# Kernel tuning notes

Hardware: AMD Instinct MI355X
Metric: run time of the kernel (lower is better)

The kernel has to match this reference:

```python
import jax, jax.numpy as jnp
import numpy as np

B, T, D = 2, 1024, 1024
E, H, TOPK = 32, 256, 4
S, HS = 2, H * TOPK  # shared experts, shared hidden dim


def setup_inputs() -> dict:
    key = jax.random.key(0)
    ks = jax.random.split(key, 10)
    sc = 0.02
    return {
        "x": jax.random.normal(ks[0], (B, T, D), dtype=jnp.float32),
        "Wr": jax.random.normal(ks[1], (E, D), dtype=jnp.float32) * sc,
        "router_bias": jnp.zeros((E,), dtype=jnp.float32),
        "Wg": jax.random.normal(ks[2], (E, H, D), dtype=jnp.float32) * sc,
        "Wu": jax.random.normal(ks[3], (E, H, D), dtype=jnp.float32) * sc,
        "Wd": jax.random.normal(ks[4], (E, D, H), dtype=jnp.float32) * sc,
        "Sg": jax.random.normal(ks[5], (S, HS, D), dtype=jnp.float32) * sc,
        "Su": jax.random.normal(ks[6], (S, HS, D), dtype=jnp.float32) * sc,
        "Sd": jax.random.normal(ks[7], (S, D, HS), dtype=jnp.float32) * sc,
    }


def reference(x, Wr, router_bias, Wg, Wu, Wd, Sg, Su, Sd):
    Bx, Tx, Dx = x.shape
    flat = x.reshape(-1, Dx)                      # [N, D]
    N = flat.shape[0]

    # Router: softmax over raw logits, top-k selection on biased logits
    logits = flat @ Wr.T                          # [N, E]
    scores = jax.nn.softmax(logits, axis=-1)
    _, topk_idx = jax.lax.top_k(logits + router_bias, TOPK)   # [N, K]
    topk_scores = jnp.take_along_axis(scores, topk_idx, axis=-1)
    topk_scores = topk_scores / jnp.sum(topk_scores, axis=-1, keepdims=True)

    # Dense per-token per-expert combine weights (0 for unselected experts)
    cw = jnp.zeros((N, E), dtype=flat.dtype).at[
        jnp.arange(N)[:, None], topk_idx
    ].add(topk_scores)                            # [N, E]

    # Routed experts: SwiGLU applied per expert, zero-weighted if unselected
    g = jnp.einsum("nd,ehd->neh", flat, Wg)       # [N, E, H]
    u = jnp.einsum("nd,ehd->neh", flat, Wu)
    h = jax.nn.silu(g) * u
    hw = h * cw[:, :, None]                       # fold combine weight before down-proj
    out = jnp.einsum("neh,edh->nd", hw, Wd)       # [N, D]

    # Shared experts: always active, summed on top
    gs = jnp.einsum("nd,shd->nsh", flat, Sg)      # [N, S, HS]
    us = jnp.einsum("nd,shd->nsh", flat, Su)
    hs = jax.nn.silu(gs) * us
    out = out + jnp.einsum("nsh,sdh->nd", hs, Sd)

    return out.reshape(Bx, Tx, Dx)
```

## Files before the change

kernel.cpp:

```cpp
#include <hip/hip_runtime.h>
#include <hip/hip_bf16.h>


#define N_TOK 2048
#define DDIM 1024
#define NEXP 32
#define HDIM 256
#define TOPK 4
#define NSH 2
#define HSH 1024
#define CNTS 32
#define WMAX 160

typedef unsigned short us4 __attribute__((ext_vector_type(4)));
typedef unsigned short us8 __attribute__((ext_vector_type(8)));
typedef short bf16x8 __attribute__((ext_vector_type(8)));
typedef float f32x4 __attribute__((ext_vector_type(4)));

__device__ __forceinline__ unsigned short f2bf(float f) {
  union { float f; unsigned u; } v; v.f = f;
  unsigned r = v.u + 0x7fffu + ((v.u >> 16) & 1u);
  return (unsigned short)(r >> 16);
}
__device__ __forceinline__ float bf2f(unsigned short h) {
  union { unsigned u; float f; } v; v.u = ((unsigned)h) << 16; return v.f;
}
__device__ __forceinline__ uint2 cvt4u(float4 v) {
  union { __hip_bfloat162 b; unsigned u; } a, b2;
  a.b  = __float22bfloat162_rn(make_float2(v.x, v.y));
  b2.b = __float22bfloat162_rn(make_float2(v.z, v.w));
  return make_uint2(a.u, b2.u);
}

__device__ __forceinline__ void pipe_barrier() {
  asm volatile("s_waitcnt lgkmcnt(0)" ::: "memory");
  __builtin_amdgcn_s_barrier();
  __builtin_amdgcn_sched_barrier(0);
}

#define C_X4   524288L
#define C_WG4  2621440L
#define C_WU4  4718592L
#define C_WD4  6815744L
#define C_SG4  7340032L
#define C_SU4  7864320L
#define C_TOT4 8388608L
#define NCVT   16384

__global__ __launch_bounds__(256) void k_prep(const float* __restrict__ x,
                                              const float* __restrict__ Wr,
                                              const float* __restrict__ rb,
                                              const float* __restrict__ Wg,
                                              const float* __restrict__ Wu,
                                              const float* __restrict__ Wd,
                                              const float* __restrict__ Sg,
                                              const float* __restrict__ Su,
                                              const float* __restrict__ Sd,
                                              unsigned short* __restrict__ xb,
                                              unsigned short* __restrict__ Wgb,
                                              unsigned short* __restrict__ Wub,
                                              unsigned short* __restrict__ Wdb,
                                              unsigned short* __restrict__ Sgb,
                                              unsigned short* __restrict__ Sub,
                                              unsigned short* __restrict__ Sdb,
                                              int* __restrict__ cnt,
                                              int* __restrict__ ent,
                                              float* __restrict__ wgt) {
  __shared__ float sX[8 * 1024];
  __shared__ float sLog[8 * 32];
  int tid = threadIdx.x;
  if (blockIdx.x >= 256) {
    long base = (long)(blockIdx.x - 256) * 512;
    const float* s; unsigned short* d; long off;
    if (base < C_WG4) {
      if (base < C_X4)  { s = x;  d = xb;  off = base; }
      else              { s = Wg; d = Wgb; off = base - C_X4; }
    } else if (base < C_WD4) {
      if (base < C_WU4) { s = Wu; d = Wub; off = base - C_WG4; }
      else              { s = Wd; d = Wdb; off = base - C_WU4; }
    } else if (base < C_SU4) {
      if (base < C_SG4) { s = Sg; d = Sgb; off = base - C_WD4; }
      else              { s = Su; d = Sub; off = base - C_SG4; }
    } else              { s = Sd; d = Sdb; off = base - C_SU4; }
    long i0 = off + tid;
    long i1 = i0 + 256;
    float4 v0 = reinterpret_cast<const float4*>(s)[i0];
    float4 v1 = reinterpret_cast<const float4*>(s)[i1];
    reinterpret_cast<uint2*>(d)[i0] = cvt4u(v0);
    reinterpret_cast<uint2*>(d)[i1] = cvt4u(v1);
    return;
  }
  int blk = blockIdx.x;
  {
    const float4* xsrc = reinterpret_cast<const float4*>(x + (size_t)blk * 8 * 1024);
    float4* xdst = reinterpret_cast<float4*>(sX);
#pragma unroll
    for (int i = 0; i < 8; i++) xdst[tid + 256 * i] = xsrc[tid + 256 * i];
  }
  __syncthreads();
  int tloc = tid >> 5, e = tid & 31;
  const float4* wr4 = reinterpret_cast<const float4*>(Wr + (size_t)e * DDIM);
  const float* xr = sX + tloc * 1024;
  float acc = 0.f;
#pragma unroll 8
  for (int d4 = 0; d4 < 256; d4++) {
    float4 wv = wr4[d4];
    acc += xr[d4 * 4 + 0] * wv.x + xr[d4 * 4 + 1] * wv.y +
           xr[d4 * 4 + 2] * wv.z + xr[d4 * 4 + 3] * wv.w;
  }
  sLog[tloc * 32 + e] = acc;
  __syncthreads();
  if (tid < 8) {
    int tok = blk * 8 + tid;
    const float* lg = sLog + tid * 32;
    int usedmask = 0;
    int idx[TOPK]; float lv[TOPK];
#pragma unroll
    for (int k = 0; k < TOPK; k++) {
      float best = -3.4e38f; int bi = 0;
      for (int ee = 0; ee < NEXP; ee++) {
        if ((usedmask >> ee) & 1) continue;
        float v = lg[ee] + rb[ee];
        if (v > best) { best = v; bi = ee; }
      }
      usedmask |= 1 << bi; idx[k] = bi; lv[k] = lg[bi];
    }
    float m = fmaxf(fmaxf(lv[0], lv[1]), fmaxf(lv[2], lv[3]));
    float w[TOPK]; float ssum = 0.f;
#pragma unroll
    for (int k = 0; k < TOPK; k++) { w[k] = __expf(lv[k] - m); ssum += w[k]; }
    float inv = 1.f / ssum;
#pragma unroll
    for (int k = 0; k < TOPK; k++) {
      int ee = idx[k];
      int pos = atomicAdd(&cnt[ee * CNTS], 1);
      ent[ee * N_TOK + pos] = tok * TOPK + k;
      wgt[ee * N_TOK + pos] = w[k] * inv;
    }
  }
}

__global__ void k_plan(const int* __restrict__ cnt, int* __restrict__ wk, int* __restrict__ nwk) {
  if (threadIdx.x != 0) return;
  int w = 0;
  for (int e = 0; e < NEXP; e++) {
    int ne = cnt[e * CNTS];
    int nt = (ne + 63) >> 6;
    for (int t = 0; t < nt; t++) wk[w++] = e | (t << 8);
  }
  nwk[0] = w;
}

__global__ __launch_bounds__(256) void k_routed_gu(const unsigned short* __restrict__ xb,
                                                   const unsigned short* __restrict__ Wgb,
                                                   const unsigned short* __restrict__ Wub,
                                                   const int* __restrict__ cnt,
                                                   const int* __restrict__ ent,
                                                   const float* __restrict__ wgt,
                                                   unsigned short* __restrict__ hw,
                                                   const int* __restrict__ wk,
                                                   const int* __restrict__ nwk) {
  int widx = blockIdx.x;
  if (widx >= nwk[0]) return;
  int item = wk[widx];
  int e = item & 255, mt = item >> 8, ht = blockIdx.y;
  int ne = cnt[e * CNTS];
  __shared__ unsigned short sA[2][64 * 40];
  __shared__ unsigned short sB[2][128 * 40];
  __shared__ int sTok[64];
  __shared__ float sW[64];
  int tid = threadIdx.x, lane = tid & 63, w = tid >> 6;
  if (tid < 64) {
    int pos = mt * 64 + tid;
    int p2 = min(pos, ne - 1);
    sTok[tid] = ent[e * N_TOK + p2];
    sW[tid] = (pos < ne) ? wgt[e * N_TOK + p2] : 0.f;
  }
  __syncthreads();

  int arow = tid >> 2, akc = tid & 3;
  const unsigned short* aSrc = xb + (size_t)(sTok[arow] >> 2) * DDIM + akc * 8;
  int aOff = arow * 40 + akc * 8;
  const unsigned short* bSrc[2];
  int bOff[2];
#pragma unroll
  for (int p = 0; p < 2; p++) {
    int c = tid + p * 256;
    int row = c >> 2, kc = c & 3;
    int sel = (row >> 4) & 1;
    int h = ht * 64 + ((row >> 5) << 4) + (row & 15);
    bSrc[p] = (sel ? Wub : Wgb) + (size_t)(e * HDIM + h) * DDIM + kc * 8;
    bOff[p] = row * 40 + kc * 8;
  }

  us8 aReg = *reinterpret_cast<const us8*>(aSrc);
  us8 bReg[2];
#pragma unroll
  for (int p = 0; p < 2; p++) bReg[p] = *reinterpret_cast<const us8*>(bSrc[p]);

  f32x4 acc[8];
#pragma unroll
  for (int f = 0; f < 8; f++) acc[f] = {0.f, 0.f, 0.f, 0.f};

  int cur = 0;
  for (int step = 0; step < 32; ++step) {
    *reinterpret_cast<us8*>(&sA[cur][aOff]) = aReg;
#pragma unroll
    for (int p = 0; p < 2; p++) *reinterpret_cast<us8*>(&sB[cur][bOff[p]]) = bReg[p];
    if (step < 31) {
      int k0 = (step + 1) * 32;
      aReg = *reinterpret_cast<const us8*>(aSrc + k0);
#pragma unroll
      for (int p = 0; p < 2; p++) bReg[p] = *reinterpret_cast<const us8*>(bSrc[p] + k0);
    }
    pipe_barrier();
    int ka = (lane >> 4) * 8;
    bf16x8 a = *reinterpret_cast<const bf16x8*>(&sA[cur][(w * 16 + (lane & 15)) * 40 + ka]);
#pragma unroll
    for (int f = 0; f < 8; f++) {
      bf16x8 b = *reinterpret_cast<const bf16x8*>(&sB[cur][(f * 16 + (lane & 15)) * 40 + ka]);
      acc[f] = __builtin_amdgcn_mfma_f32_16x16x32_bf16(a, b, acc[f], 0, 0, 0);
    }
    cur ^= 1;
  }
#pragma unroll
  for (int j = 0; j < 4; j++) {
#pragma unroll
    for (int r = 0; r < 4; r++) {
      int tl = w * 16 + ((lane >> 4) << 2) + r;
      int pos = mt * 64 + tl;
      if (pos < ne) {
        float g = acc[2 * j][r], u = acc[2 * j + 1][r];
        float hval = (g / (1.f + __expf(-g))) * u * sW[tl];
        int ts = sTok[tl];
        int h = ht * 64 + j * 16 + (lane & 15);
        hw[(size_t)ts * HDIM + h] = f2bf(hval);
      }
    }
  }
}

__global__ __launch_bounds__(256) void k_routed_down(const unsigned short* __restrict__ hw,
                                                     const unsigned short* __restrict__ Wdb,
                                                     const int* __restrict__ cnt,
                                                     const int* __restrict__ ent,
                                                     unsigned short* __restrict__ Pslot,
                                                     const int* __restrict__ wk,
                                                     const int* __restrict__ nwk) {
  int widx = blockIdx.x;
  if (widx >= nwk[0]) return;
  int item = wk[widx];
  int e = item & 255, mt = item >> 8, dh = blockIdx.y;
  int ne = cnt[e * CNTS];
  __shared__ unsigned short sA[2][64 * 40];
  __shared__ unsigned short sB[2][256 * 40];
  __shared__ int sTok[64];
  int tid = threadIdx.x, lane = tid & 63, w = tid >> 6;
  if (tid < 64) {
    int pos = mt * 64 + tid;
    int p2 = min(pos, ne - 1);
    sTok[tid] = ent[e * N_TOK + p2];
  }
  __syncthreads();

  int arow = tid >> 2, akc = tid & 3;
  const unsigned short* aSrc = hw + (size_t)sTok[arow] * HDIM + akc * 8;
  int aOff = arow * 40 + akc * 8;
  const unsigned short* bSrc[4];
  int bOff[4];
#pragma unroll
  for (int p = 0; p < 4; p++) {
    int c = tid + p * 256;
    int row = c >> 2, kc = c & 3;
    int d = dh * 256 + row;
    bSrc[p] = Wdb + (size_t)(e * DDIM + d) * HDIM + kc * 8;
    bOff[p] = row * 40 + kc * 8;
  }

  us8 aReg = *reinterpret_cast<const us8*>(aSrc);
  us8 bReg[4];
#pragma unroll
  for (int p = 0; p < 4; p++) bReg[p] = *reinterpret_cast<const us8*>(bSrc[p]);

  f32x4 acc[16];
#pragma unroll
  for (int f = 0; f < 16; f++) acc[f] = {0.f, 0.f, 0.f, 0.f};

  int cur = 0;
  for (int step = 0; step < 8; ++step) {
    *reinterpret_cast<us8*>(&sA[cur][aOff]) = aReg;
#pragma unroll
    for (int p = 0; p < 4; p++) *reinterpret_cast<us8*>(&sB[cur][bOff[p]]) = bReg[p];
    if (step < 7) {
      int k0 = (step + 1) * 32;
      aReg = *reinterpret_cast<const us8*>(aSrc + k0);
#pragma unroll
      for (int p = 0; p < 4; p++) bReg[p] = *reinterpret_cast<const us8*>(bSrc[p] + k0);
    }
    pipe_barrier();
    int ka = (lane >> 4) * 8;
    bf16x8 a = *reinterpret_cast<const bf16x8*>(&sA[cur][(w * 16 + (lane & 15)) * 40 + ka]);
#pragma unroll
    for (int f = 0; f < 16; f++) {
      bf16x8 b = *reinterpret_cast<const bf16x8*>(&sB[cur][(f * 16 + (lane & 15)) * 40 + ka]);
      acc[f] = __builtin_amdgcn_mfma_f32_16x16x32_bf16(a, b, acc[f], 0, 0, 0);
    }
    cur ^= 1;
  }
#pragma unroll
  for (int f = 0; f < 16; f++) {
#pragma unroll
    for (int r = 0; r < 4; r++) {
      int tl = w * 16 + ((lane >> 4) << 2) + r;
      int pos = mt * 64 + tl;
      if (pos < ne) {
        int ts = sTok[tl];
        int d = dh * 256 + f * 16 + (lane & 15);
        Pslot[(size_t)ts * DDIM + d] = f2bf(acc[f][r]);
      }
    }
  }
}

__global__ __launch_bounds__(512) void k_shared_gu(const unsigned short* __restrict__ xb,
                                                   const unsigned short* __restrict__ Sgb,
                                                   const unsigned short* __restrict__ Sub,
                                                   unsigned short* __restrict__ hs) {
  int s = blockIdx.x >> 3, ht = blockIdx.x & 7;
  int mt = blockIdx.y;
  __shared__ unsigned short sA[2][128 * 40];
  __shared__ unsigned short sB[2][256 * 40];
  int tid = threadIdx.x, lane = tid & 63, wid = tid >> 6;
  int wm = wid >> 2, wn = wid & 3;

  int ar = tid >> 2, akc = tid & 3;
  const unsigned short* aSrc = xb + (size_t)(mt * 128 + ar) * DDIM + akc * 8;
  int aOff = ar * 40 + akc * 8;
  const unsigned short* bSrc[2];
  int bOff[2];
#pragma unroll
  for (int p = 0; p < 2; p++) {
    int c = tid + p * 512;
    int row = c >> 2, kc = c & 3;
    int sel = (row >> 4) & 1;
    int h = ht * 128 + ((row >> 5) << 4) + (row & 15);
    bSrc[p] = (sel ? Sub : Sgb) + (size_t)(s * HSH + h) * DDIM + kc * 8;
    bOff[p] = row * 40 + kc * 8;
  }

  us8 aReg = *reinterpret_cast<const us8*>(aSrc);
  us8 bReg[2];
#pragma unroll
  for (int p = 0; p < 2; p++) bReg[p] = *reinterpret_cast<const us8*>(bSrc[p]);

  f32x4 acc[4][4];
#pragma unroll
  for (int mf = 0; mf < 4; mf++)
#pragma unroll
    for (int nf = 0; nf < 4; nf++) acc[mf][nf] = {0.f, 0.f, 0.f, 0.f};

  int cur = 0;
  for (int step = 0; step < 32; ++step) {
    *reinterpret_cast<us8*>(&sA[cur][aOff]) = aReg;
#pragma unroll
    for (int p = 0; p < 2; p++) *reinterpret_cast<us8*>(&sB[cur][bOff[p]]) = bReg[p];
    if (step < 31) {
      int k0 = (step + 1) * 32;
      aReg = *reinterpret_cast<const us8*>(aSrc + k0);
#pragma unroll
      for (int p = 0; p < 2; p++) bReg[p] = *reinterpret_cast<const us8*>(bSrc[p] + k0);
    }
    pipe_barrier();
    int ka = (lane >> 4) * 8;
    bf16x8 a[4];
#pragma unroll
    for (int mf = 0; mf < 4; mf++)
      a[mf] = *reinterpret_cast<const bf16x8*>(&sA[cur][(wm * 64 + mf * 16 + (lane & 15)) * 40 + ka]);
#pragma unroll
    for (int nf = 0; nf < 4; nf++) {
      bf16x8 b = *reinterpret_cast<const bf16x8*>(&sB[cur][(wn * 64 + nf * 16 + (lane & 15)) * 40 + ka]);
#pragma unroll
      for (int mf = 0; mf < 4; mf++)
        acc[mf][nf] = __builtin_amdgcn_mfma_f32_16x16x32_bf16(a[mf], b, acc[mf][nf], 0, 0, 0);
    }
    cur ^= 1;
  }
#pragma unroll
  for (int mf = 0; mf < 4; mf++) {
#pragma unroll
    for (int t = 0; t < 2; t++) {
#pragma unroll
      for (int r = 0; r < 4; r++) {
        int tok = mt * 128 + wm * 64 + mf * 16 + ((lane >> 4) << 2) + r;
        float g = acc[mf][2 * t][r], u = acc[mf][2 * t + 1][r];
        float hval = (g / (1.f + __expf(-g))) * u;
        int h = ht * 128 + (wn * 2 + t) * 16 + (lane & 15);
        hs[(size_t)(tok * NSH + s) * HSH + h] = f2bf(hval);
      }
    }
  }
}

__global__ __launch_bounds__(512) void k_shared_down(const unsigned short* __restrict__ hs,
                                                     const unsigned short* __restrict__ Sdb,
                                                     unsigned short* __restrict__ Psh) {
  int dh = blockIdx.x >> 1, s = blockIdx.x & 1;
  int mt = blockIdx.y;
  __shared__ unsigned short sA[2][128 * 40];
  __shared__ unsigned short sB[2][128 * 40];
  int tid = threadIdx.x, lane = tid & 63, wid = tid >> 6;
  int wm = wid >> 2, wn = wid & 3;

  int ar = tid >> 2, akc = tid & 3;
  const unsigned short* aSrc = hs + (size_t)((mt * 128 + ar) * NSH + s) * HSH + akc * 8;
  int aOff = ar * 40 + akc * 8;
  int br = tid >> 2, bkc = tid & 3;
  const unsigned short* bSrc = Sdb + (size_t)(s * DDIM + dh * 128 + br) * HSH + bkc * 8;
  int bOff = br * 40 + bkc * 8;

  us8 aReg = *reinterpret_cast<const us8*>(aSrc);
  us8 bReg = *reinterpret_cast<const us8*>(bSrc);

  f32x4 acc[4][2];
#pragma unroll
  for (int mf = 0; mf < 4; mf++)
#pragma unroll
    for (int nf = 0; nf < 2; nf++) acc[mf][nf] = {0.f, 0.f, 0.f, 0.f};

  int cur = 0;
  for (int step = 0; step < 32; ++step) {
    *reinterpret_cast<us8*>(&sA[cur][aOff]) = aReg;
    *reinterpret_cast<us8*>(&sB[cur][bOff]) = bReg;
    if (step < 31) {
      int k0 = (step + 1) * 32;
      aReg = *reinterpret_cast<const us8*>(aSrc + k0);
      bReg = *reinterpret_cast<const us8*>(bSrc + k0);
    }
    pipe_barrier();
    int ka = (lane >> 4) * 8;
    bf16x8 a[4];
#pragma unroll
    for (int mf = 0; mf < 4; mf++)
      a[mf] = *reinterpret_cast<const bf16x8*>(&sA[cur][(wm * 64 + mf * 16 + (lane & 15)) * 40 + ka]);
#pragma unroll
    for (int nf = 0; nf < 2; nf++) {
      bf16x8 b = *reinterpret_cast<const bf16x8*>(&sB[cur][(wn * 32 + nf * 16 + (lane & 15)) * 40 + ka]);
#pragma unroll
      for (int mf = 0; mf < 4; mf++)
        acc[mf][nf] = __builtin_amdgcn_mfma_f32_16x16x32_bf16(a[mf], b, acc[mf][nf], 0, 0, 0);
    }
    cur ^= 1;
  }
#pragma unroll
  for (int mf = 0; mf < 4; mf++) {
#pragma unroll
    for (int nf = 0; nf < 2; nf++) {
#pragma unroll
      for (int r = 0; r < 4; r++) {
        int tok = mt * 128 + wm * 64 + mf * 16 + ((lane >> 4) << 2) + r;
        int d = dh * 128 + wn * 32 + nf * 16 + (lane & 15);
        Psh[(size_t)s * N_TOK * DDIM + (size_t)tok * DDIM + d] = f2bf(acc[mf][nf][r]);
      }
    }
  }
}

__global__ __launch_bounds__(256) void k_combine(const unsigned short* __restrict__ Pslot,
                                                 const unsigned short* __restrict__ Psh,
                                                 float* __restrict__ out) {
  int i = blockIdx.x * 256 + threadIdx.x;
  int base = i * 8;
  int tok = base >> 10, d = base & 1023;
  const us8 p0 = *reinterpret_cast<const us8*>(Pslot + ((size_t)tok * 4 + 0) * DDIM + d);
  const us8 p1 = *reinterpret_cast<const us8*>(Pslot + ((size_t)tok * 4 + 1) * DDIM + d);
  const us8 p2 = *reinterpret_cast<const us8*>(Pslot + ((size_t)tok * 4 + 2) * DDIM + d);
  const us8 p3 = *reinterpret_cast<const us8*>(Pslot + ((size_t)tok * 4 + 3) * DDIM + d);
  const us8 q0 = *reinterpret_cast<const us8*>(Psh + (size_t)base);
  const us8 q1 = *reinterpret_cast<const us8*>(Psh + (size_t)N_TOK * DDIM + base);
  float o[8];
#pragma unroll
  for (int j = 0; j < 8; j++)
    o[j] = bf2f(p0[j]) + bf2f(p1[j]) + bf2f(p2[j]) + bf2f(p3[j]) + bf2f(q0[j]) + bf2f(q1[j]);
  float4 v0 = {o[0], o[1], o[2], o[3]};
  float4 v1 = {o[4], o[5], o[6], o[7]};
  reinterpret_cast<float4*>(out + base)[0] = v0;
  reinterpret_cast<float4*>(out + base)[1] = v1;
}

extern "C" void kernel_launch(void* const* d_in, const int* in_sizes, int n_in,
                              void* d_out, int out_size, void* d_ws, size_t ws_size,
                              hipStream_t stream) {
  const float* x  = (const float*)d_in[0];
  const float* Wr = (const float*)d_in[1];
  const float* rb = (const float*)d_in[2];
  const float* Wg = (const float*)d_in[3];
  const float* Wu = (const float*)d_in[4];
  const float* Wd = (const float*)d_in[5];
  const float* Sg = (const float*)d_in[6];
  const float* Su = (const float*)d_in[7];
  const float* Sd = (const float*)d_in[8];
  float* out = (float*)d_out;
  char* w = (char*)d_ws;

  unsigned short* xb    = (unsigned short*)(w + (size_t)0);
  unsigned short* Wgb   = (unsigned short*)(w + ((size_t)4  << 20));
  unsigned short* Wub   = (unsigned short*)(w + ((size_t)20 << 20));
  unsigned short* Wdb   = (unsigned short*)(w + ((size_t)36 << 20));
  unsigned short* Sgb   = (unsigned short*)(w + ((size_t)52 << 20));
  unsigned short* Sub   = (unsigned short*)(w + ((size_t)56 << 20));
  unsigned short* Sdb   = (unsigned short*)(w + ((size_t)60 << 20));
  unsigned short* hw    = (unsigned short*)(w + ((size_t)64 << 20));
  unsigned short* hs    = (unsigned short*)(w + ((size_t)68 << 20));
  unsigned short* Pslot = (unsigned short*)(w + ((size_t)76 << 20));
  unsigned short* Psh   = (unsigned short*)(w + ((size_t)92 << 20));
  int*   cnt = (int*)(w + ((size_t)100 << 20));
  int*   ent = (int*)(w + ((size_t)100 << 20) + 8192);
  float* wgt = (float*)(w + ((size_t)100 << 20) + 8192 + (size_t)NEXP * N_TOK * 4);
  int*   wk  = (int*)(w + ((size_t)102 << 20));
  int*   nwk = (int*)(w + ((size_t)102 << 20) + 4096);

  hipMemsetAsync(cnt, 0, NEXP * CNTS * sizeof(int), stream);

  k_prep<<<256 + NCVT, 256, 0, stream>>>(x, Wr, rb, Wg, Wu, Wd, Sg, Su, Sd,
                                         xb, Wgb, Wub, Wdb, Sgb, Sub, Sdb,
                                         cnt, ent, wgt);
  k_plan<<<1, 64, 0, stream>>>(cnt, wk, nwk);

  k_routed_gu<<<dim3(WMAX, 4), 256, 0, stream>>>(xb, Wgb, Wub, cnt, ent, wgt, hw, wk, nwk);
  k_routed_down<<<dim3(WMAX, 4), 256, 0, stream>>>(hw, Wdb, cnt, ent, Pslot, wk, nwk);

  k_shared_gu<<<dim3(16, 16), 512, 0, stream>>>(xb, Sgb, Sub, hs);
  k_shared_down<<<dim3(16, 16), 512, 0, stream>>>(hs, Sdb, Psh);

  k_combine<<<N_TOK * DDIM / (256 * 8), 256, 0, stream>>>(Pslot, Psh, out);
}
```

Measured before the change: 169.2 us.

## Use 128-row tiles with 512 threads in routed gate/up GEMM; split router blocks

The routed gate/up kernel now uses 128-token tiles and 512 threads, with an 8-wave layout where each wave computes a 64x32 sub-tile. This reuses each weight tile across twice as many tokens and raises the number of MFMAs per LDS fragment load. A second work list with 128-row granularity is built in k_plan. The router part of k_prep now handles 4 tokens per block instead of 8, giving twice as many blocks, and only 128 threads compute logits. Larger tiles mean more padding waste for experts with few tokens and fewer blocks in flight.

```diff
diff --git a/kernel.cpp b/kernel.cpp
--- a/kernel.cpp
+++ b/kernel.cpp
@@ -11,6 +11,7 @@
 #define HSH 1024
 #define CNTS 32
 #define WMAX 160
+#define WM2  96
 
 typedef unsigned short us4 __attribute__((ext_vector_type(4)));
 typedef unsigned short us8 __attribute__((ext_vector_type(8)));
@@ -45,6 +46,7 @@
 #define C_SG4  7340032L
 #define C_SU4  7864320L
 #define C_TOT4 8388608L
+#define NRTR   512
 #define NCVT   16384
 
 __global__ __launch_bounds__(256) void k_prep(const float* __restrict__ x,
@@ -66,11 +68,11 @@
                                               int* __restrict__ cnt,
                                               int* __restrict__ ent,
                                               float* __restrict__ wgt) {
-  __shared__ float sX[8 * 1024];
-  __shared__ float sLog[8 * 32];
+  __shared__ float sX[4 * 1024];
+  __shared__ float sLog[4 * 32];
   int tid = threadIdx.x;
-  if (blockIdx.x >= 256) {
-    long base = (long)(blockIdx.x - 256) * 512;
+  if (blockIdx.x >= NRTR) {
+    long base = (long)(blockIdx.x - NRTR) * 512;
     const float* s; unsigned short* d; long off;
     if (base < C_WG4) {
       if (base < C_X4)  { s = x;  d = xb;  off = base; }
@@ -92,26 +94,28 @@
   }
   int blk = blockIdx.x;
   {
-    const float4* xsrc = reinterpret_cast<const float4*>(x + (size_t)blk * 8 * 1024);
+    const float4* xsrc = reinterpret_cast<const float4*>(x + (size_t)blk * 4 * 1024);
     float4* xdst = reinterpret_cast<float4*>(sX);
 #pragma unroll
-    for (int i = 0; i < 8; i++) xdst[tid + 256 * i] = xsrc[tid + 256 * i];
+    for (int i = 0; i < 4; i++) xdst[tid + 256 * i] = xsrc[tid + 256 * i];
   }
   __syncthreads();
-  int tloc = tid >> 5, e = tid & 31;
-  const float4* wr4 = reinterpret_cast<const float4*>(Wr + (size_t)e * DDIM);
-  const float* xr = sX + tloc * 1024;
-  float acc = 0.f;
+  if (tid < 128) {
+    int tloc = tid >> 5, e = tid & 31;
+    const float4* wr4 = reinterpret_cast<const float4*>(Wr + (size_t)e * DDIM);
+    const float* xr = sX + tloc * 1024;
+    float acc = 0.f;
 #pragma unroll 8
-  for (int d4 = 0; d4 < 256; d4++) {
-    float4 wv = wr4[d4];
-    acc += xr[d4 * 4 + 0] * wv.x + xr[d4 * 4 + 1] * wv.y +
-           xr[d4 * 4 + 2] * wv.z + xr[d4 * 4 + 3] * wv.w;
-  }
-  sLog[tloc * 32 + e] = acc;
+    for (int d4 = 0; d4 < 256; d4++) {
+      float4 wv = wr4[d4];
+      acc += xr[d4 * 4 + 0] * wv.x + xr[d4 * 4 + 1] * wv.y +
+             xr[d4 * 4 + 2] * wv.z + xr[d4 * 4 + 3] * wv.w;
+    }
+    sLog[tloc * 32 + e] = acc;
+  }
   __syncthreads();
-  if (tid < 8) {
-    int tok = blk * 8 + tid;
+  if (tid < 4) {
+    int tok = blk * 4 + tid;
     const float* lg = sLog + tid * 32;
     int usedmask = 0;
     int idx[TOPK]; float lv[TOPK];
@@ -140,101 +144,103 @@
   }
 }
 
-__global__ void k_plan(const int* __restrict__ cnt, int* __restrict__ wk, int* __restrict__ nwk) {
+__global__ void k_plan(const int* __restrict__ cnt, int* __restrict__ wk, int* __restrict__ nwk,
+                       int* __restrict__ wk2, int* __restrict__ nwk2) {
   if (threadIdx.x != 0) return;
-  int w = 0;
+  int w = 0, w2 = 0;
   for (int e = 0; e < NEXP; e++) {
     int ne = cnt[e * CNTS];
     int nt = (ne + 63) >> 6;
     for (int t = 0; t < nt; t++) wk[w++] = e | (t << 8);
+    int nt2 = (ne + 127) >> 7;
+    for (int t = 0; t < nt2; t++) wk2[w2++] = e | (t << 8);
   }
   nwk[0] = w;
-}
-
-__global__ __launch_bounds__(256) void k_routed_gu(const unsigned short* __restrict__ xb,
+  nwk2[0] = w2;
+}
+
+__global__ __launch_bounds__(512) void k_routed_gu(const unsigned short* __restrict__ xb,
                                                    const unsigned short* __restrict__ Wgb,
                                                    const unsigned short* __restrict__ Wub,
                                                    const int* __restrict__ cnt,
                                                    const int* __restrict__ ent,
                                                    const float* __restrict__ wgt,
                                                    unsigned short* __restrict__ hw,
-                                                   const int* __restrict__ wk,
-                                                   const int* __restrict__ nwk) {
+                                                   const int* __restrict__ wk2,
+                                                   const int* __restrict__ nwk2) {
   int widx = blockIdx.x;
-  if (widx >= nwk[0]) return;
-  int item = wk[widx];
+  if (widx >= nwk2[0]) return;
+  int item = wk2[widx];
   int e = item & 255, mt = item >> 8, ht = blockIdx.y;
   int ne = cnt[e * CNTS];
-  __shared__ unsigned short sA[2][64 * 40];
+  __shared__ unsigned short sA[2][128 * 40];
   __shared__ unsigned short sB[2][128 * 40];
-  __shared__ int sTok[64];
-  __shared__ float sW[64];
-  int tid = threadIdx.x, lane = tid & 63, w = tid >> 6;
-  if (tid < 64) {
-    int pos = mt * 64 + tid;
+  __shared__ int sTok[128];
+  __shared__ float sW[128];
+  int tid = threadIdx.x, lane = tid & 63, wid = tid >> 6;
+  int wm = wid >> 2, wn = wid & 3;
+  if (tid < 128) {
+    int pos = mt * 128 + tid;
     int p2 = min(pos, ne - 1);
     sTok[tid] = ent[e * N_TOK + p2];
     sW[tid] = (pos < ne) ? wgt[e * N_TOK + p2] : 0.f;
   }
   __syncthreads();
 
-  int arow = tid >> 2, akc = tid & 3;
-  const unsigned short* aSrc = xb + (size_t)(sTok[arow] >> 2) * DDIM + akc * 8;
-  int aOff = arow * 40 + akc * 8;
-  const unsigned short* bSrc[2];
-  int bOff[2];
-#pragma unroll
-  for (int p = 0; p < 2; p++) {
-    int c = tid + p * 256;
-    int row = c >> 2, kc = c & 3;
-    int sel = (row >> 4) & 1;
-    int h = ht * 64 + ((row >> 5) << 4) + (row & 15);
-    bSrc[p] = (sel ? Wub : Wgb) + (size_t)(e * HDIM + h) * DDIM + kc * 8;
-    bOff[p] = row * 40 + kc * 8;
-  }
+  int ar = tid >> 2, akc = tid & 3;
+  const unsigned short* aSrc = xb + (size_t)(sTok[ar] >> 2) * DDIM + akc * 8;
+  int aOff = ar * 40 + akc * 8;
+  int br = tid >> 2, bkc = tid & 3;
+  int sel = (br >> 4) & 1;
+  int h = ht * 64 + ((br >> 5) << 4) + (br & 15);
+  const unsigned short* bSrc = (sel ? Wub : Wgb) + (size_t)(e * HDIM + h) * DDIM + bkc * 8;
+  int bOff = br * 40 + bkc * 8;
 
   us8 aReg = *reinterpret_cast<const us8*>(aSrc);
-  us8 bReg[2];
-#pragma unroll
-  for (int p = 0; p < 2; p++) bReg[p] = *reinterpret_cast<const us8*>(bSrc[p]);
-
-  f32x4 acc[8];
-#pragma unroll
-  for (int f = 0; f < 8; f++) acc[f] = {0.f, 0.f, 0.f, 0.f};
+  us8 bReg = *reinterpret_cast<const us8*>(bSrc);
+
+  f32x4 acc[4][2];
+#pragma unroll
+  for (int mf = 0; mf < 4; mf++)
+#pragma unroll
+    for (int nf = 0; nf < 2; nf++) acc[mf][nf] = {0.f, 0.f, 0.f, 0.f};
 
   int cur = 0;
   for (int step = 0; step < 32; ++step) {
     *reinterpret_cast<us8*>(&sA[cur][aOff]) = aReg;
-#pragma unroll
-    for (int p = 0; p < 2; p++) *reinterpret_cast<us8*>(&sB[cur][bOff[p]]) = bReg[p];
+    *reinterpret_cast<us8*>(&sB[cur][bOff]) = bReg;
     if (step < 31) {
       int k0 = (step + 1) * 32;
       aReg = *reinterpret_cast<const us8*>(aSrc + k0);
-#pragma unroll
-      for (int p = 0; p < 2; p++) bReg[p] = *reinterpret_cast<const us8*>(bSrc[p] + k0);
+      bReg = *reinterpret_cast<const us8*>(bSrc + k0);
     }
     pipe_barrier();
     int ka = (lane >> 4) * 8;
-    bf16x8 a = *reinterpret_cast<const bf16x8*>(&sA[cur][(w * 16 + (lane & 15)) * 40 + ka]);
-#pragma unroll
-    for (int f = 0; f < 8; f++) {
-      bf16x8 b = *reinterpret_cast<const bf16x8*>(&sB[cur][(f * 16 + (lane & 15)) * 40 + ka]);
-      acc[f] = __builtin_amdgcn_mfma_f32_16x16x32_bf16(a, b, acc[f], 0, 0, 0);
+    bf16x8 a[4];
+#pragma unroll
+    for (int mf = 0; mf < 4; mf++)
+      a[mf] = *reinterpret_cast<const bf16x8*>(&sA[cur][(wm * 64 + mf * 16 + (lane & 15)) * 40 + ka]);
+#pragma unroll
+    for (int nf = 0; nf < 2; nf++) {
+      bf16x8 b = *reinterpret_cast<const bf16x8*>(&sB[cur][(wn * 32 + nf * 16 + (lane & 15)) * 40 + ka]);
+#pragma unroll
+      for (int mf = 0; mf < 4; mf++)
+        acc[mf][nf] = __builtin_amdgcn_mfma_f32_16x16x32_bf16(a[mf], b, acc[mf][nf], 0, 0, 0);
     }
     cur ^= 1;
   }
 #pragma unroll
-  for (int j = 0; j < 4; j++) {
+  for (int mf = 0; mf < 4; mf++) {
 #pragma unroll
     for (int r = 0; r < 4; r++) {
-      int tl = w * 16 + ((lane >> 4) << 2) + r;
-      int pos = mt * 64 + tl;
+      int tl = wm * 64 + mf * 16 + ((lane >> 4) << 2) + r;
+      int pos = mt * 128 + tl;
       if (pos < ne) {
-        float g = acc[2 * j][r], u = acc[2 * j + 1][r];
+        float g = acc[mf][0][r], u = acc[mf][1][r];
         float hval = (g / (1.f + __expf(-g))) * u * sW[tl];
         int ts = sTok[tl];
-        int h = ht * 64 + j * 16 + (lane & 15);
-        hw[(size_t)ts * HDIM + h] = f2bf(hval);
+        int hcol = ht * 64 + wn * 16 + (lane & 15);
+        hw[(size_t)ts * HDIM + hcol] = f2bf(hval);
       }
     }
   }
@@ -516,17 +522,19 @@
   int*   cnt = (int*)(w + ((size_t)100 << 20));
   int*   ent = (int*)(w + ((size_t)100 << 20) + 8192);
   float* wgt = (float*)(w + ((size_t)100 << 20) + 8192 + (size_t)NEXP * N_TOK * 4);
-  int*   wk  = (int*)(w + ((size_t)102 << 20));
-  int*   nwk = (int*)(w + ((size_t)102 << 20) + 4096);
+  int*   wk   = (int*)(w + ((size_t)102 << 20));
+  int*   nwk  = (int*)(w + ((size_t)102 << 20) + 4096);
+  int*   wk2  = (int*)(w + ((size_t)102 << 20) + 8192);
+  int*   nwk2 = (int*)(w + ((size_t)102 << 20) + 12288);
 
   hipMemsetAsync(cnt, 0, NEXP * CNTS * sizeof(int), stream);
 
-  k_prep<<<256 + NCVT, 256, 0, stream>>>(x, Wr, rb, Wg, Wu, Wd, Sg, Su, Sd,
-                                         xb, Wgb, Wub, Wdb, Sgb, Sub, Sdb,
-                                         cnt, ent, wgt);
-  k_plan<<<1, 64, 0, stream>>>(cnt, wk, nwk);
-
-  k_routed_gu<<<dim3(WMAX, 4), 256, 0, stream>>>(xb, Wgb, Wub, cnt, ent, wgt, hw, wk, nwk);
+  k_prep<<<NRTR + NCVT, 256, 0, stream>>>(x, Wr, rb, Wg, Wu, Wd, Sg, Su, Sd,
+                                          xb, Wgb, Wub, Wdb, Sgb, Sub, Sdb,
+                                          cnt, ent, wgt);
+  k_plan<<<1, 64, 0, stream>>>(cnt, wk, nwk, wk2, nwk2);
+
+  k_routed_gu<<<dim3(WM2, 4), 512, 0, stream>>>(xb, Wgb, Wub, cnt, ent, wgt, hw, wk2, nwk2);
   k_routed_down<<<dim3(WMAX, 4), 256, 0, stream>>>(hw, Wdb, cnt, ent, Pslot, wk, nwk);
 
   k_shared_gu<<<dim3(16, 16), 512, 0, stream>>>(xb, Sgb, Sub, hs);
```

Result: no change. 170.8 us (+0.9%).
